# Kernel optimization log

Measured on AMD Instinct MI355X. Metric: run time of the kernel, lower is better.

Reference implementation:

```python
import jax, jax.numpy as jnp
import numpy as np

TEMPERATURE = 0.1
EPS = 1e-8  # torch F.cosine_similarity default eps

def setup_inputs() -> dict:
    key = jax.random.key(0)
    features = jax.random.normal(key, (8192, 1024), dtype=jnp.float32)
    return {"features": features}

def reference(features):
    B = features.shape[0] // 2
    z1 = features[:B]  # [B, D]
    z2 = features[B:]  # [B, D]
    # cosine similarity: normalize each row (clamped norm like torch eps) then GEMM
    n1 = jnp.maximum(jnp.linalg.norm(z1, axis=-1, keepdims=True), EPS)
    n2 = jnp.maximum(jnp.linalg.norm(z2, axis=-1, keepdims=True), EPS)
    logits = jnp.einsum('id,jd->ij', z1 / n1, z2 / n2) / TEMPERATURE  # [B, B]
    # cross-entropy with labels = arange(B): mean of -log_softmax diagonal
    logp = jax.nn.log_softmax(logits, axis=-1)
    loss = -jnp.mean(jnp.diagonal(logp))
    return loss
```

## Files before the change

kernel.cpp:

```cpp
#include <hip/hip_runtime.h>
#include <hip/hip_bf16.h>

typedef __attribute__((ext_vector_type(4))) int i32x4;

#define D 1024
#define NROWS 4096
#define SCALE_U 14.426950408889634f
#define LN2 0.69314718055994530942f
#define LSE_SHIFT 16.0f
#define NCC 32
#define BM 128
#define BKE 64
#define NSLAB 16


__device__ __forceinline__ void gload16(const void* g, void* l) {
    __builtin_amdgcn_global_load_lds((const __attribute__((address_space(1))) void*)g,
                                     (__attribute__((address_space(3))) void*)l, 16, 0, 0);
}

__global__ __launch_bounds__(256) void nrm_kernel(const float* __restrict__ feat,
                                                  signed char* __restrict__ zn,
                                                  float* __restrict__ fs) {
    const int row = blockIdx.x;
    const int tid = threadIdx.x;
    const float4 v = reinterpret_cast<const float4*>(feat + (size_t)row * D)[tid];
    float ss = v.x * v.x + v.y * v.y + v.z * v.z + v.w * v.w;
    float am = fmaxf(fmaxf(fabsf(v.x), fabsf(v.y)), fmaxf(fabsf(v.z), fabsf(v.w)));
#pragma unroll
    for (int off = 32; off > 0; off >>= 1) {
        ss += __shfl_down(ss, off);
        am = fmaxf(am, __shfl_down(am, off));
    }
    __shared__ float reds[4], redm[4];
    const int lane = tid & 63, wid = tid >> 6;
    if (lane == 0) { reds[wid] = ss; redm[wid] = am; }
    __syncthreads();
    const float tot = reds[0] + reds[1] + reds[2] + reds[3];
    const float amx = fmaxf(fmaxf(redm[0], redm[1]), fmaxf(redm[2], redm[3]));
    const float nrm = fmaxf(sqrtf(tot), 1e-8f);
    const float wmax = fmaxf(amx / nrm, 1e-12f);
    const float qs = 127.0f / (wmax * nrm);
    int q0 = (int)rintf(fminf(fmaxf(v.x * qs, -127.f), 127.f));
    int q1 = (int)rintf(fminf(fmaxf(v.y * qs, -127.f), 127.f));
    int q2 = (int)rintf(fminf(fmaxf(v.z * qs, -127.f), 127.f));
    int q3 = (int)rintf(fminf(fmaxf(v.w * qs, -127.f), 127.f));
    const int packed = (q0 & 255) | ((q1 & 255) << 8) | ((q2 & 255) << 16) | (q3 << 24);
    reinterpret_cast<int*>(zn)[(size_t)row * (D / 4) + tid] = packed;
    if (tid == 0)
        fs[row] = ((row < NROWS) ? SCALE_U : 1.0f) * wmax * (1.0f / 127.0f);
}

__global__ __launch_bounds__(256, 4) void gram_lse_kernel(const signed char* __restrict__ zn,
                                                          const float* __restrict__ fs,
                                                          float* __restrict__ psum,
                                                          float* __restrict__ diag) {
    __shared__ __align__(16) signed char As[BM * BKE];
    __shared__ __align__(16) signed char Bs[BM * BKE];
    __shared__ float sbuf[BM][2];

    const int bid = blockIdx.x;
    const int xcd = bid & 7, t = bid >> 3;
    const int rt = (xcd >> 2) * 16 + (t >> 3);
    const int cc = (xcd & 3) * 8 + (t & 7);

    const int tid = threadIdx.x;
    const int lane = tid & 63;
    const int wid  = tid >> 6;
    const int wm = wid >> 1, wn = wid & 1;
    const int l15 = lane & 15, g = lane >> 4;

    const int lrow = lane >> 2;
    const int j16  = (lane & 3) * 16;
    const signed char* gA = zn + (size_t)(rt * BM + lrow) * D + j16;
    const signed char* gB = zn + (size_t)(NROWS + cc * BM + lrow) * D + j16;

    i32x4 acc[4][4];
#pragma unroll
    for (int i = 0; i < 4; i++)
#pragma unroll
        for (int j = 0; j < 4; j++) acc[i][j] = (i32x4){0, 0, 0, 0};

    for (int kb = 0; kb < NSLAB; ++kb) {
        __syncthreads();
#pragma unroll
        for (int it = 0; it < 2; ++it) {
            const int r0 = (wid * 2 + it) * 16;
            gload16(gA + (size_t)r0 * D + kb * BKE, &As[r0 * BKE]);
            gload16(gB + (size_t)r0 * D + kb * BKE, &Bs[r0 * BKE]);
        }
        __syncthreads();

        i32x4 b[4];
#pragma unroll
        for (int fn = 0; fn < 4; ++fn)
            b[fn] = *reinterpret_cast<const i32x4*>(&Bs[(wn * 64 + fn * 16 + l15) * BKE + g * 16]);
#pragma unroll
        for (int fr = 0; fr < 4; ++fr) {
            const i32x4 a = *reinterpret_cast<const i32x4*>(&As[(wm * 64 + fr * 16 + l15) * BKE + g * 16]);
#pragma unroll
            for (int fn = 0; fn < 4; ++fn)
                acc[fr][fn] = __builtin_amdgcn_mfma_i32_16x16x64_i8(a, b[fn], acc[fr][fn], 0, 0, 0);
        }
    }

    float fs2[4];
#pragma unroll
    for (int fn = 0; fn < 4; ++fn)
        fs2[fn] = fs[NROWS + cc * BM + wn * 64 + fn * 16 + l15];

#pragma unroll
    for (int fr = 0; fr < 4; ++fr) {
#pragma unroll
        for (int r = 0; r < 4; ++r) {
            const int rl = wm * 64 + fr * 16 + g * 4 + r;
            const float f1 = fs[rt * BM + rl];
            float s = 0.f;
#pragma unroll
            for (int fn = 0; fn < 4; ++fn) {
                const float u = f1 * fs2[fn] * (float)acc[fr][fn][r];
                s += exp2f(u - LSE_SHIFT);
                if (rt == cc && rl == wn * 64 + fn * 16 + l15)
                    diag[rt * BM + rl] = u;
            }
#pragma unroll
            for (int off = 1; off < 16; off <<= 1) s += __shfl_xor(s, off);
            if (l15 == 0) sbuf[rl][wn] = s;
        }
    }
    __syncthreads();
    if (tid < BM) {
        psum[(size_t)(rt * BM + tid) * NCC + cc] = sbuf[tid][0] + sbuf[tid][1];
    }
}

__global__ __launch_bounds__(256) void rowfinal_kernel(const float* __restrict__ psum,
                                                       const float* __restrict__ diag,
                                                       float* __restrict__ contrib) {
    const int i = blockIdx.x * 256 + threadIdx.x;
    float4 ps[8];
#pragma unroll
    for (int q = 0; q < 8; ++q)
        ps[q] = reinterpret_cast<const float4*>(psum + (size_t)i * NCC)[q];
    float s = 0.f;
#pragma unroll
    for (int q = 0; q < 8; ++q) s += (ps[q].x + ps[q].y) + (ps[q].z + ps[q].w);
    contrib[i] = LSE_SHIFT + log2f(s) - diag[i];
}

__global__ __launch_bounds__(256) void final_kernel(const float* __restrict__ contrib,
                                                    float* __restrict__ out) {
    const int tid = threadIdx.x;
    float s = 0.f;
    for (int j = tid; j < NROWS; j += 256) s += contrib[j];
#pragma unroll
    for (int off = 32; off > 0; off >>= 1) s += __shfl_down(s, off);
    __shared__ float red[4];
    const int lane = tid & 63, wid = tid >> 6;
    if (lane == 0) red[wid] = s;
    __syncthreads();
    if (tid == 0) out[0] = (red[0] + red[1] + red[2] + red[3]) * (LN2 / (float)NROWS);
}

extern "C" void kernel_launch(void* const* d_in, const int* in_sizes, int n_in,
                              void* d_out, int out_size, void* d_ws, size_t ws_size,
                              hipStream_t stream) {
    const float* feat = (const float*)d_in[0];
    signed char* zn = (signed char*)d_ws;
    float* fs      = (float*)((char*)d_ws + 8388608);
    float* psum    = (float*)((char*)d_ws + 8421376);
    float* diag    = (float*)((char*)d_ws + 8945664);
    float* contrib = (float*)((char*)d_ws + 8962048);
    float* out = (float*)d_out;

    nrm_kernel<<<8192, 256, 0, stream>>>(feat, zn, fs);
    gram_lse_kernel<<<1024, 256, 0, stream>>>(zn, fs, psum, diag);
    rowfinal_kernel<<<16, 256, 0, stream>>>(psum, diag, contrib);
    final_kernel<<<1, 256, 0, stream>>>(contrib, out);
}
```

Before: 47.18 us.

## Double-buffer LDS tiles in int8 gram kernel with XOR-swizzled layout

The int8 GEMM main loop now uses two LDS buffers per operand. It issues the global-to-LDS load for the next K slab before running the MFMAs on the current one, and keeps only one barrier per iteration. The LDS layout is also rearranged with an XOR swizzle on 16-byte chunks, which is meant to reduce bank conflicts on the fragment reads. The aim is to hide global-load latency behind compute, at the cost of doubling LDS use per block, which may limit occupancy.

```diff
diff --git a/kernel.cpp b/kernel.cpp
--- a/kernel.cpp
+++ b/kernel.cpp
@@ -55,8 +55,8 @@
                                                           const float* __restrict__ fs,
                                                           float* __restrict__ psum,
                                                           float* __restrict__ diag) {
-    __shared__ __align__(16) signed char As[BM * BKE];
-    __shared__ __align__(16) signed char Bs[BM * BKE];
+    __shared__ __align__(16) signed char As[2][64 * 128];
+    __shared__ __align__(16) signed char Bs[2][64 * 128];
     __shared__ float sbuf[BM][2];
 
     const int bid = blockIdx.x;
@@ -70,10 +70,23 @@
     const int wm = wid >> 1, wn = wid & 1;
     const int l15 = lane & 15, g = lane >> 4;
 
-    const int lrow = lane >> 2;
-    const int j16  = (lane & 3) * 16;
-    const signed char* gA = zn + (size_t)(rt * BM + lrow) * D + j16;
-    const signed char* gB = zn + (size_t)(NROWS + cc * BM + lrow) * D + j16;
+    const int srl    = lane >> 3;
+    const int sidx   = (lane & 7) ^ srl;
+    const int srow   = srl * 2 + (sidx >> 2);
+    const int schunk = (sidx & 3) * 16;
+    const signed char* gA = zn + (size_t)(rt * BM + srow) * D + schunk;
+    const signed char* gB = zn + (size_t)(NROWS + cc * BM + srow) * D + schunk;
+
+    const int aoff = (wm * 32 + (l15 >> 1)) * 128 + ((((l15 & 1) << 2) | g) ^ (l15 >> 1)) * 16;
+    const int boff = (wn * 32 + (l15 >> 1)) * 128 + ((((l15 & 1) << 2) | g) ^ (l15 >> 1)) * 16;
+
+#define STAGE(buf, kb) do {                                                        \
+    _Pragma("unroll")                                                              \
+    for (int it = 0; it < 2; ++it) {                                               \
+        const int r0 = wid * 2 + it;                  \
+        gload16(gA + (size_t)(r0 * 16) * D + (size_t)(kb) * BKE, &As[buf][r0 * 1024]); \
+        gload16(gB + (size_t)(r0 * 16) * D + (size_t)(kb) * BKE, &Bs[buf][r0 * 1024]); \
+    } } while (0)
 
     i32x4 acc[4][4];
 #pragma unroll
@@ -81,28 +94,30 @@
 #pragma unroll
         for (int j = 0; j < 4; j++) acc[i][j] = (i32x4){0, 0, 0, 0};
 
-    for (int kb = 0; kb < NSLAB; ++kb) {
+#define COMPUTE(buf) do {                                                          \
+    i32x4 b[4];                                                                    \
+    _Pragma("unroll")                                                              \
+    for (int fn = 0; fn < 4; ++fn)                                                 \
+        b[fn] = *reinterpret_cast<const i32x4*>(&Bs[buf][boff + fn * 1024]);       \
+    _Pragma("unroll")                                                              \
+    for (int fr = 0; fr < 4; ++fr) {                                               \
+        const i32x4 a = *reinterpret_cast<const i32x4*>(&As[buf][aoff + fr * 1024]); \
+        _Pragma("unroll")                                                          \
+        for (int fn = 0; fn < 4; ++fn)                                             \
+            acc[fr][fn] = __builtin_amdgcn_mfma_i32_16x16x64_i8(a, b[fn], acc[fr][fn], 0, 0, 0); \
+    } } while (0)
+
+    STAGE(0, 0);
+    __syncthreads();
+    for (int kb = 0; kb < NSLAB - 1; ++kb) {
+        const int cur = kb & 1;
+        STAGE(cur ^ 1, kb + 1);
+        COMPUTE(cur);
         __syncthreads();
-#pragma unroll
-        for (int it = 0; it < 2; ++it) {
-            const int r0 = (wid * 2 + it) * 16;
-            gload16(gA + (size_t)r0 * D + kb * BKE, &As[r0 * BKE]);
-            gload16(gB + (size_t)r0 * D + kb * BKE, &Bs[r0 * BKE]);
-        }
-        __syncthreads();
-
-        i32x4 b[4];
-#pragma unroll
-        for (int fn = 0; fn < 4; ++fn)
-            b[fn] = *reinterpret_cast<const i32x4*>(&Bs[(wn * 64 + fn * 16 + l15) * BKE + g * 16]);
-#pragma unroll
-        for (int fr = 0; fr < 4; ++fr) {
-            const i32x4 a = *reinterpret_cast<const i32x4*>(&As[(wm * 64 + fr * 16 + l15) * BKE + g * 16]);
-#pragma unroll
-            for (int fn = 0; fn < 4; ++fn)
-                acc[fr][fn] = __builtin_amdgcn_mfma_i32_16x16x64_i8(a, b[fn], acc[fr][fn], 0, 0, 0);
-        }
     }
+    COMPUTE((NSLAB - 1) & 1);
+#undef STAGE
+#undef COMPUTE
 
     float fs2[4];
 #pragma unroll
```

Result: no change. 47.34 us (+0.3%).
